# Performance work log

Measured on AMD Instinct MI355X. Metric: run time of the kernel, lower is better.

The kernel has to match this reference:

```python
import jax, jax.numpy as jnp
import numpy as np

EPSILON = 0.1  # init kwarg epsilon
Q = 1          # init kwarg q (norm order for W1 rows)
N_HIDDEN1 = 4096


def setup_inputs() -> dict:
    key = jax.random.key(0)
    k1, k2, k3, k4 = jax.random.split(key, 4)
    B, I, H, O = 64, 1024, 4096, 256
    gamma = 1.0
    x = jax.random.normal(k1, (B, I), dtype=jnp.float32)
    y = jax.random.randint(k2, (B, O), 0, 2)  # int labels, cast to float in forward
    W1 = -jax.random.uniform(k3, (H, I), dtype=jnp.float32) / (gamma * H)
    W2 = jax.random.uniform(k4, (O, H), dtype=jnp.float32) / (gamma * O)
    bias1 = jnp.zeros((H,), dtype=jnp.float32)
    bias2 = jnp.zeros((O,), dtype=jnp.float32)
    return {"x": x, "y": y, "W1": W1, "W2": W2, "bias1": bias1, "bias2": bias2}


def reference(x, y, W1, W2, bias1, bias2):
    # adv=True branch of AdvOneLayer.forward, fully vectorized.
    # W1_norm[j] = ||W1[j, :]||_q with q=1
    W1_norm = jnp.sum(jnp.abs(W1), axis=1)  # [H]
    yf = y.astype(jnp.float32)               # [B, O]
    # pert[b, i, j] = -eps * y[b, i] * sign(W2[i, j]) * W1_norm[j]
    pert = -EPSILON * yf[:, :, None] * jnp.sign(W2)[None, :, :] * W1_norm[None, None, :]  # [B, O, H]
    # NOTE: the original also computes hidden1 = relu(x @ W1[j] + bias1[j] + pert)
    # inside the loop, but hidden1 is never used (dead code); the stored summand
    # is output[b, i, j] = W2[i, j] * n_hidden1, independent of x and the batch.
    output = jnp.broadcast_to((W2 * N_HIDDEN1)[None, :, :], pert.shape)  # [B, O, H]
    nn_output = jnp.sum(output, axis=2) + bias2  # [B, O]
    return nn_output, pert
```

## Files before the change

kernel.cpp:

```cpp
#include <hip/hip_runtime.h>

#define BB 64
#define II 1024
#define HH 4096
#define OO 256
#define EPSI 0.1f

__global__ __launch_bounds__(256) void prep_kernel(
    const float* __restrict__ W1, const float* __restrict__ W2,
    const float* __restrict__ bias2,
    float* __restrict__ nscaled, float* __restrict__ nnrow) {
  const int bid = blockIdx.x;
  const int tid = threadIdx.x;
  __shared__ float red[4];

  float s = 0.0f;
  if (bid < HH) {
    const float4* row = (const float4*)(W1 + (size_t)bid * II);
    float4 v = row[tid];
    s = fabsf(v.x) + fabsf(v.y) + fabsf(v.z) + fabsf(v.w);
  } else {
    const int o = bid - HH;
    const float4* row = (const float4*)(W2 + (size_t)o * HH);
#pragma unroll
    for (int k = 0; k < 4; ++k) {
      float4 v = row[tid + 256 * k];
      s += v.x + v.y + v.z + v.w;
    }
  }

#pragma unroll
  for (int off = 32; off > 0; off >>= 1) s += __shfl_down(s, off);
  if ((tid & 63) == 0) red[tid >> 6] = s;
  __syncthreads();
  if (tid == 0) {
    float t = red[0] + red[1] + red[2] + red[3];
    if (bid < HH) {
      nscaled[bid] = -EPSI * t;
    } else {
      const int o = bid - HH;
      nnrow[o] = 4096.0f * t + bias2[o];
    }
  }
}

__global__ __launch_bounds__(256) void write_kernel(
    const int* __restrict__ y, const float* __restrict__ W2,
    const float* __restrict__ nscaled, const float* __restrict__ nnrow,
    float* __restrict__ out) {
  const int r = blockIdx.x;
  const int o = r & (OO - 1);
  const int tid = threadIdx.x;

  if (tid == 0) out[r] = nnrow[o];

  float4* dst = (float4*)(out + (size_t)BB * OO + (size_t)r * HH);
  const int yv = y[r];

  if (yv == 0) {
    const float4 z = {0.f, 0.f, 0.f, 0.f};
#pragma unroll
    for (int k = 0; k < 4; ++k) dst[tid + 256 * k] = z;
  } else {
    const float4* w  = (const float4*)(W2 + (size_t)o * HH);
    const float4* ns = (const float4*)nscaled;
#pragma unroll
    for (int k = 0; k < 4; ++k) {
      float4 wv = w[tid + 256 * k];
      float4 nv = ns[tid + 256 * k];
      float4 p;
      p.x = nv.x * ((wv.x > 0.f) ? 1.f : ((wv.x < 0.f) ? -1.f : 0.f));
      p.y = nv.y * ((wv.y > 0.f) ? 1.f : ((wv.y < 0.f) ? -1.f : 0.f));
      p.z = nv.z * ((wv.z > 0.f) ? 1.f : ((wv.z < 0.f) ? -1.f : 0.f));
      p.w = nv.w * ((wv.w > 0.f) ? 1.f : ((wv.w < 0.f) ? -1.f : 0.f));
      dst[tid + 256 * k] = p;
    }
  }
}

extern "C" void kernel_launch(void* const* d_in, const int* in_sizes, int n_in,
                              void* d_out, int out_size, void* d_ws, size_t ws_size,
                              hipStream_t stream) {
  const int*   y     = (const int*)d_in[1];
  const float* W1    = (const float*)d_in[2];
  const float* W2    = (const float*)d_in[3];
  const float* bias2 = (const float*)d_in[5];
  float* out = (float*)d_out;

  float* nscaled = (float*)d_ws;
  float* nnrow   = nscaled + HH;

  prep_kernel<<<HH + OO, 256, 0, stream>>>(W1, W2, bias2, nscaled, nnrow);
  write_kernel<<<BB * OO, 256, 0, stream>>>(y, W2, nscaled, nnrow, out);
}
```

Baseline: 295.2 us.

## Reuse sign-scaled W2 row across batch chunk with nontemporal stores

```diff
diff --git a/kernel.cpp b/kernel.cpp
--- a/kernel.cpp
+++ b/kernel.cpp
@@ -5,14 +5,18 @@
 #define HH 4096
 #define OO 256
 #define EPSI 0.1f
+#define BCHUNK 8
+
+typedef float vf4 __attribute__((ext_vector_type(4)));
 
 __global__ __launch_bounds__(256) void prep_kernel(
     const float* __restrict__ W1, const float* __restrict__ W2,
     const float* __restrict__ bias2,
-    float* __restrict__ nscaled, float* __restrict__ nnrow) {
+    float* __restrict__ nscaled, float* __restrict__ out) {
   const int bid = blockIdx.x;
   const int tid = threadIdx.x;
   __shared__ float red[4];
+  __shared__ float bval;
 
   float s = 0.0f;
   if (bid < HH) {
@@ -38,42 +42,47 @@
     if (bid < HH) {
       nscaled[bid] = -EPSI * t;
     } else {
-      const int o = bid - HH;
-      nnrow[o] = 4096.0f * t + bias2[o];
+      bval = 4096.0f * t + bias2[bid - HH];
     }
+  }
+  if (bid >= HH) {
+    __syncthreads();
+    if (tid < BB) out[(size_t)tid * OO + (bid - HH)] = bval;
   }
 }
 
 __global__ __launch_bounds__(256) void write_kernel(
     const int* __restrict__ y, const float* __restrict__ W2,
-    const float* __restrict__ nscaled, const float* __restrict__ nnrow,
-    float* __restrict__ out) {
-  const int r = blockIdx.x;
-  const int o = r & (OO - 1);
+    const float* __restrict__ nscaled, float* __restrict__ out) {
+  const int o  = blockIdx.x & (OO - 1);
+  const int bc = blockIdx.x >> 8;
   const int tid = threadIdx.x;
 
-  if (tid == 0) out[r] = nnrow[o];
+  const float4* w  = (const float4*)(W2 + (size_t)o * HH);
+  const float4* ns = (const float4*)nscaled;
 
-  float4* dst = (float4*)(out + (size_t)BB * OO + (size_t)r * HH);
-  const int yv = y[r];
+  vf4 sv[4];
+#pragma unroll
+  for (int k = 0; k < 4; ++k) {
+    float4 wv = w[tid + 256 * k];
+    float4 nv = ns[tid + 256 * k];
+    sv[k].x = nv.x * ((wv.x > 0.f) ? 1.f : ((wv.x < 0.f) ? -1.f : 0.f));
+    sv[k].y = nv.y * ((wv.y > 0.f) ? 1.f : ((wv.y < 0.f) ? -1.f : 0.f));
+    sv[k].z = nv.z * ((wv.z > 0.f) ? 1.f : ((wv.z < 0.f) ? -1.f : 0.f));
+    sv[k].w = nv.w * ((wv.w > 0.f) ? 1.f : ((wv.w < 0.f) ? -1.f : 0.f));
+  }
 
-  if (yv == 0) {
-    const float4 z = {0.f, 0.f, 0.f, 0.f};
+  float* pert = out + (size_t)BB * OO;
 #pragma unroll
-    for (int k = 0; k < 4; ++k) dst[tid + 256 * k] = z;
-  } else {
-    const float4* w  = (const float4*)(W2 + (size_t)o * HH);
-    const float4* ns = (const float4*)nscaled;
+  for (int i = 0; i < BCHUNK; ++i) {
+    const int b = bc * BCHUNK + i;
+    const int r = b * OO + o;
+    const float yf = (float)y[r];
+    vf4* dst = (vf4*)(pert + (size_t)r * HH);
 #pragma unroll
     for (int k = 0; k < 4; ++k) {
-      float4 wv = w[tid + 256 * k];
-      float4 nv = ns[tid + 256 * k];
-      float4 p;
-      p.x = nv.x * ((wv.x > 0.f) ? 1.f : ((wv.x < 0.f) ? -1.f : 0.f));
-      p.y = nv.y * ((wv.y > 0.f) ? 1.f : ((wv.y < 0.f) ? -1.f : 0.f));
-      p.z = nv.z * ((wv.z > 0.f) ? 1.f : ((wv.z < 0.f) ? -1.f : 0.f));
-      p.w = nv.w * ((wv.w > 0.f) ? 1.f : ((wv.w < 0.f) ? -1.f : 0.f));
-      dst[tid + 256 * k] = p;
+      vf4 p = sv[k] * yf;
+      __builtin_nontemporal_store(p, &dst[tid + 256 * k]);
     }
   }
 }
@@ -88,8 +97,7 @@
   float* out = (float*)d_out;
 
   float* nscaled = (float*)d_ws;
-  float* nnrow   = nscaled + HH;
 
-  prep_kernel<<<HH + OO, 256, 0, stream>>>(W1, W2, bias2, nscaled, nnrow);
-  write_kernel<<<BB * OO, 256, 0, stream>>>(y, W2, nscaled, nnrow, out);
+  prep_kernel<<<HH + OO, 256, 0, stream>>>(W1, W2, bias2, nscaled, out);
+  write_kernel<<<OO * (BB / BCHUNK), 256, 0, stream>>>(y, W2, nscaled, out);
 }
```

After: 288.7 us. 1.02x faster.
